# Performance work log

Hardware: AMD Instinct MI355X
Metric: run time of the kernel (lower is better)

The kernel has to match this reference:

```python
import jax, jax.numpy as jnp
import numpy as np

D = 1024      # d_model
E = 8         # num_experts
K = 2         # top_k
H = 4096      # expert_dim (bottleneck)
P = 256       # proj_dim
BATCH, SEQ = 2, 2048
CLAMP_MAX = float(np.log(1.0 / 0.01))
INIT_T = 0.5


def setup_inputs() -> dict:
    key = jax.random.key(0)
    ks = jax.random.split(key, 6)
    x = jax.random.normal(ks[0], (BATCH, SEQ, D), jnp.float32)
    # cosine projector (nn.Linear default init ~ U(-1/sqrt(D), 1/sqrt(D)))
    lim = 1.0 / np.sqrt(D)
    Wp = jax.random.uniform(ks[1], (P, D), jnp.float32, -lim, lim)
    bp = jnp.zeros((P,), jnp.float32)
    sim = 0.01 * jax.random.normal(ks[2], (P, E), jnp.float32)
    temp = jnp.full((1,), np.log(1.0 / INIT_T), jnp.float32)
    # RepAdapter 1x1 convs == linear layers; xavier_uniform, zero bias
    bA = float(np.sqrt(6.0 / (D + H)))
    A = jax.random.uniform(ks[3], (E, H, D), jnp.float32, -bA, bA)
    a_bias = jnp.zeros((E, H), jnp.float32)
    Bw = jax.random.uniform(ks[4], (E, D, H), jnp.float32, -bA, bA)
    b_bias = jnp.zeros((E, D), jnp.float32)
    return dict(x=x, Wp=Wp, bp=bp, sim=sim, temp=temp, A=A, a_bias=a_bias, Bw=Bw, b_bias=b_bias)


def reference(x, Wp, bp, sim, temp, A, a_bias, Bw, b_bias):
    B, S, d = x.shape
    e = sim.shape[1]
    xf = x.reshape(-1, d)                                  # [T, D]
    # cosine gate
    proj = xf @ Wp.T + bp                                  # [T, P]
    projn = proj / jnp.maximum(jnp.linalg.norm(proj, axis=1, keepdims=True), 1e-12)
    simn = sim / jnp.maximum(jnp.linalg.norm(sim, axis=0, keepdims=True), 1e-12)
    scale = jnp.exp(jnp.minimum(temp, CLAMP_MAX))          # [1]
    gate_probs = jax.nn.softmax((projn @ simn) * scale, axis=-1)   # [T, E]
    topv, topi = jax.lax.top_k(gate_probs, K)              # [T, K]
    topv = topv / (topv.sum(axis=-1, keepdims=True) + 1e-8)
    # per-token per-expert combine weight
    w = jnp.sum(topv[:, :, None] * jax.nn.one_hot(topi, e, dtype=x.dtype), axis=1)  # [T, E]

    # experts: y_e(x) = x + B_e(A_e x + a_e) + b_e (no nonlinearity); combine weighted
    def body(acc, params):
        Ae, ab, Be, bb, we = params
        h = xf @ Ae.T + ab                                 # [T, H]
        f = h @ Be.T + bb                                  # [T, D]
        return acc + we[:, None] * (xf + f), None

    out, _ = jax.lax.scan(body, jnp.zeros_like(xf), (A, a_bias, Bw, b_bias, w.T))
    out = out.reshape(B, S, d)

    frac = gate_probs.mean(axis=0)                         # expert_fractions
    aux_loss = jnp.sum((frac - 1.0 / e) ** 2)
    usage = jnp.bincount(topi.reshape(-1), length=e).astype(jnp.float32)
    return out, aux_loss, frac, usage
```

## Files before the change

kernel.cpp:

```cpp
#include <hip/hip_runtime.h>
#include <stdint.h>


typedef __attribute__((ext_vector_type(4))) float floatx4;
typedef __attribute__((ext_vector_type(8))) short shortx8;
typedef unsigned short ushort_t;

#define T_TOKENS 4096
#define D_DIM    1024
#define E_EXP    8
#define H_DIM    4096
#define P_DIM    256
#define ROWS_PAD 9344
#define MBLK     73

__device__ __forceinline__ ushort_t f2bf(float f) {
  union { float f; unsigned int u; } c; c.f = f;
  unsigned int u = c.u;
  unsigned int r = u + 0x7FFFu + ((u >> 16) & 1u);
  return (ushort_t)(r >> 16);
}

__device__ __forceinline__ void stage16(const ushort_t* g, ushort_t* l) {
  __builtin_amdgcn_global_load_lds(
      (__attribute__((address_space(1))) void*)(uintptr_t)g,
      (__attribute__((address_space(3))) void*)l, 16, 0, 0);
}

__global__ __launch_bounds__(256) void k_cvt(const float* __restrict__ src,
                                             ushort_t* __restrict__ dst, int n4) {
  int g = blockIdx.x * 256 + threadIdx.x;
  if (g >= n4) return;
  floatx4 v = ((const floatx4*)src)[g];
  ushort4 o; o.x = f2bf(v.x); o.y = f2bf(v.y); o.z = f2bf(v.z); o.w = f2bf(v.w);
  ((ushort4*)dst)[g] = o;
}

__global__ __launch_bounds__(256) void k_small_init(int* counts, int* cursor,
                                                    float* frac_sum, int* row2tok) {
  int g = blockIdx.x * 256 + threadIdx.x;
  if (g < 8) { counts[g] = 0; cursor[g] = 0; frac_sum[g] = 0.f; }
  if (g < ROWS_PAD) row2tok[g] = -1;
}

__global__ __launch_bounds__(256) void k_proj(const float* __restrict__ x,
                                              const float* __restrict__ Wp,
                                              const float* __restrict__ bp,
                                              float* __restrict__ proj) {
  __shared__ float Wc[256 * 36];
  __shared__ float Xc[16 * 36];
  int tid = threadIdx.x;
  int t0 = blockIdx.x * 16;
  int cg = tid & 31, tg = tid >> 5;
  floatx4 acc[2][8];
#pragma unroll
  for (int a = 0; a < 2; a++)
#pragma unroll
    for (int b = 0; b < 8; b++) acc[a][b] = (floatx4){0.f, 0.f, 0.f, 0.f};
  for (int kc = 0; kc < 32; ++kc) {
    int k0 = kc * 32;
    __syncthreads();
#pragma unroll
    for (int it = 0; it < 8; ++it) {
      int f = it * 256 + tid;
      int j = f >> 3, kk = (f & 7) << 2;
      floatx4 v = *(const floatx4*)(Wp + j * 1024 + k0 + kk);
      *(floatx4*)(Wc + j * 36 + kk) = v;
    }
    if (tid < 128) {
      int t = tid >> 3, kk = (tid & 7) << 2;
      floatx4 v = *(const floatx4*)(x + (size_t)(t0 + t) * 1024 + k0 + kk);
      *(floatx4*)(Xc + t * 36 + kk) = v;
    }
    __syncthreads();
#pragma unroll
    for (int k4 = 0; k4 < 8; ++k4) {
      floatx4 xv[2], wv[8];
#pragma unroll
      for (int tt = 0; tt < 2; tt++) xv[tt] = *(floatx4*)(Xc + (tg * 2 + tt) * 36 + k4 * 4);
#pragma unroll
      for (int jj = 0; jj < 8; jj++) wv[jj] = *(floatx4*)(Wc + (cg + jj * 32) * 36 + k4 * 4);
#pragma unroll
      for (int tt = 0; tt < 2; tt++)
#pragma unroll
        for (int jj = 0; jj < 8; jj++) acc[tt][jj] += xv[tt] * wv[jj];
    }
  }
#pragma unroll
  for (int tt = 0; tt < 2; tt++)
#pragma unroll
    for (int jj = 0; jj < 8; jj++) {
      floatx4 a = acc[tt][jj];
      float s = (a.x + a.y) + (a.z + a.w);
      int t = t0 + tg * 2 + tt, j = cg + jj * 32;
      proj[t * 256 + j] = s + bp[j];
    }
}

__global__ __launch_bounds__(128) void k_gate(const float* __restrict__ proj,
                                              const float* __restrict__ sim,
                                              const float* __restrict__ temp,
                                              int* __restrict__ topi, float* __restrict__ wslot,
                                              float* __restrict__ swsum,
                                              float* __restrict__ frac_sum, int* __restrict__ counts) {
  __shared__ float simT[8][256];
  __shared__ float snorm[8];
  __shared__ float fracs[8];
  __shared__ int cnts[8];
  int tid = threadIdx.x;
  for (int i = tid; i < 2048; i += 128) { int p = i >> 3, e = i & 7; simT[e][p] = sim[i]; }
  if (tid < 8) { fracs[tid] = 0.f; cnts[tid] = 0; }
  __syncthreads();
  if (tid < 8) {
    float s = 0.f;
    for (int p = 0; p < 256; p++) { float v = simT[tid][p]; s += v * v; }
    snorm[tid] = fmaxf(sqrtf(s), 1e-12f);
  }
  __syncthreads();
  int t = blockIdx.x * 128 + tid;
  floatx4 n4 = (floatx4){0.f, 0.f, 0.f, 0.f};
  floatx4 d4[8];
#pragma unroll
  for (int e = 0; e < 8; e++) d4[e] = (floatx4){0.f, 0.f, 0.f, 0.f};
  const floatx4* pr = (const floatx4*)(proj + t * 256);
  for (int k4 = 0; k4 < 64; ++k4) {
    floatx4 p = pr[k4];
    n4 += p * p;
#pragma unroll
    for (int e = 0; e < 8; e++) d4[e] += p * *(const floatx4*)(&simT[e][k4 * 4]);
  }
  float nrm = fmaxf(sqrtf((n4.x + n4.y) + (n4.z + n4.w)), 1e-12f);
  float scale = expf(fminf(temp[0], 4.6051701859880914f));
  float pe[8];
  float mx = -1e30f;
#pragma unroll
  for (int e = 0; e < 8; e++) {
    float d = (d4[e].x + d4[e].y) + (d4[e].z + d4[e].w);
    pe[e] = d / (nrm * snorm[e]) * scale;
    mx = fmaxf(mx, pe[e]);
  }
  float sum = 0.f;
#pragma unroll
  for (int e = 0; e < 8; e++) { pe[e] = expf(pe[e] - mx); sum += pe[e]; }
#pragma unroll
  for (int e = 0; e < 8; e++) pe[e] /= sum;
  int i0 = 0;
#pragma unroll
  for (int e = 1; e < 8; e++) if (pe[e] > pe[i0]) i0 = e;
  int i1 = (i0 == 0) ? 1 : 0;
#pragma unroll
  for (int e = 0; e < 8; e++) if (e != i1 && e != i0 && pe[e] > pe[i1]) i1 = e;
  float v0 = pe[i0], v1 = pe[i1];
  float s2 = v0 + v1 + 1e-8f;
  float w0 = v0 / s2, w1 = v1 / s2;
  topi[t * 2] = i0; topi[t * 2 + 1] = i1;
  wslot[t * 2] = w0; wslot[t * 2 + 1] = w1;
  swsum[t] = w0 + w1;
#pragma unroll
  for (int e = 0; e < 8; e++) atomicAdd(&fracs[e], pe[e]);
  atomicAdd(&cnts[i0], 1); atomicAdd(&cnts[i1], 1);
  __syncthreads();
  if (tid < 8) { atomicAdd(&frac_sum[tid], fracs[tid]); atomicAdd(&counts[tid], cnts[tid]); }
}

__global__ void k_scan(const int* __restrict__ counts, const float* __restrict__ frac_sum,
                       int* __restrict__ offsets, int* __restrict__ blk2e,
                       float* __restrict__ out_tail) {
  __shared__ int offs[9];
  if (threadIdx.x == 0) {
    int off = 0;
    for (int e = 0; e < 8; e++) { offs[e] = off; off += ((counts[e] + 127) >> 7) << 7; }
    offs[8] = off;
    for (int e = 0; e < 9; e++) offsets[e] = offs[e];
    float aux = 0.f;
    for (int e = 0; e < 8; e++) { float fr = frac_sum[e] / 4096.f; aux += (fr - 0.125f) * (fr - 0.125f); }
    out_tail[0] = aux;
  }
  __syncthreads();
  int tid = threadIdx.x;
  if (tid < MBLK) {
    int r = tid * 128, e = -1;
    for (int q = 0; q < 8; q++) if (r >= offs[q] && r < offs[q + 1]) e = q;
    blk2e[tid] = e;
  }
  if (tid < 8) {
    out_tail[1 + tid] = frac_sum[tid] / 4096.f;
    out_tail[9 + tid] = (float)counts[tid];
  }
}

__global__ __launch_bounds__(256) void k_assign(const int* __restrict__ topi,
                                                const float* __restrict__ wslot,
                                                const int* __restrict__ offsets,
                                                int* __restrict__ cursor,
                                                int* __restrict__ row2tok, float* __restrict__ roww) {
  int g = blockIdx.x * 256 + threadIdx.x;
  if (g >= 8192) return;
  int t = g >> 1;
  int e = topi[g];
  int pos = atomicAdd(&cursor[e], 1);
  int r = offsets[e] + pos;
  row2tok[r] = t;
  roww[r] = wslot[g];
}

__global__ __launch_bounds__(64) void k_gather(const float* __restrict__ x,
                                               const int* __restrict__ row2tok,
                                               ushort_t* __restrict__ xg) {
  int r = blockIdx.x;
  int t = row2tok[r];
  ushort4* dst = (ushort4*)(xg + (size_t)r * 1024);
  if (t < 0) {
    ushort4 z; z.x = z.y = z.z = z.w = 0;
    for (int i = threadIdx.x; i < 256; i += 64) dst[i] = z;
  } else {
    const floatx4* src = (const floatx4*)(x + (size_t)t * 1024);
    for (int i = threadIdx.x; i < 256; i += 64) {
      floatx4 v = src[i];
      ushort4 o; o.x = f2bf(v.x); o.y = f2bf(v.y); o.z = f2bf(v.z); o.w = f2bf(v.w);
      dst[i] = o;
    }
  }
}

__global__ __launch_bounds__(256) void k_init_out(const float* __restrict__ x,
                                                  const float* __restrict__ swsum,
                                                  float* __restrict__ out) {
  int g = blockIdx.x * 256 + threadIdx.x;
  float s = swsum[g >> 8];
  floatx4 v = ((const floatx4*)x)[g];
  ((floatx4*)out)[g] = v * s;
}

__global__ __launch_bounds__(256) void k_gemm(const ushort_t* __restrict__ Aop0,
                                              const ushort_t* __restrict__ Wall,
                                              const float* __restrict__ bias,
                                              const int* __restrict__ blk2e,
                                              int K, int N,
                                              ushort_t* __restrict__ hout,
                                              float* __restrict__ outp,
                                              const int* __restrict__ row2tok,
                                              const float* __restrict__ roww) {
  int e = blk2e[blockIdx.y];
  if (e < 0) return;
  int rb = blockIdx.y, nb = blockIdx.x;
  const ushort_t* Aop = Aop0 + (size_t)rb * 128 * K;
  const ushort_t* Bop = Wall + (size_t)e * N * K + (size_t)nb * 128 * K;
  __shared__ ushort_t As[4096], Bs[4096];
  int tid = threadIdx.x, lane = tid & 63, wv = tid >> 6;
  int l15 = lane & 15, q = lane >> 4;
  int wm = (wv & 1) << 6, wn = (wv >> 1) << 6;
  floatx4 acc[4][4];
#pragma unroll
  for (int i = 0; i < 4; i++)
#pragma unroll
    for (int j = 0; j < 4; j++) acc[i][j] = (floatx4){0.f, 0.f, 0.f, 0.f};
  int c0 = tid, c1 = 256 + tid;
  size_t sa0 = (size_t)(c0 >> 2) * K + ((c0 & 3) << 3);
  size_t sa1 = (size_t)(c1 >> 2) * K + ((c1 & 3) << 3);
  ushort_t* lA0 = As + wv * 512;
  ushort_t* lA1 = As + 2048 + wv * 512;
  ushort_t* lB0 = Bs + wv * 512;
  ushort_t* lB1 = Bs + 2048 + wv * 512;
  int ksteps = K >> 5;
  for (int ks = 0; ks < ksteps; ++ks) {
    const ushort_t* Ak = Aop + ks * 32;
    const ushort_t* Bk = Bop + ks * 32;
    stage16(Ak + sa0, lA0);
    stage16(Ak + sa1, lA1);
    stage16(Bk + sa0, lB0);
    stage16(Bk + sa1, lB1);
    __syncthreads();
    shortx8 af[4], bfv[4];
#pragma unroll
    for (int i = 0; i < 4; i++) af[i] = *(const shortx8*)(As + ((wm + i * 16 + l15) << 5) + (q << 3));
#pragma unroll
    for (int i = 0; i < 4; i++) bfv[i] = *(const shortx8*)(Bs + ((wn + i * 16 + l15) << 5) + (q << 3));
#pragma unroll
    for (int i = 0; i < 4; i++)
#pragma unroll
      for (int j = 0; j < 4; j++)
        acc[i][j] = __builtin_amdgcn_mfma_f32_16x16x32_bf16(af[i], bfv[j], acc[i][j], 0, 0, 0);
    __syncthreads();
  }
  const float* be = bias + (size_t)e * N + (size_t)nb * 128;
  if (hout) {
    ushort_t* hp = hout + (size_t)(rb * 128) * N + nb * 128;
#pragma unroll
    for (int j = 0; j < 4; j++) {
      int n = wn + j * 16 + l15;
      float bv = be[n];
#pragma unroll
      for (int i = 0; i < 4; i++)
#pragma unroll
        for (int r = 0; r < 4; r++) {
          int m = wm + i * 16 + (q << 2) + r;
          hp[(size_t)m * N + n] = f2bf(acc[i][j][r] + bv);
        }
    }
  } else {
#pragma unroll
    for (int j = 0; j < 4; j++) {
      int n = wn + j * 16 + l15;
      float bv = be[n];
#pragma unroll
      for (int i = 0; i < 4; i++)
#pragma unroll
        for (int r = 0; r < 4; r++) {
          int m = wm + i * 16 + (q << 2) + r;
          int grow = rb * 128 + m;
          int tok = row2tok[grow];
          if (tok >= 0) {
            float v = (acc[i][j][r] + bv) * roww[grow];
            atomicAdd(outp + (size_t)tok * 1024 + nb * 128 + n, v);
          }
        }
    }
  }
}

extern "C" void kernel_launch(void* const* d_in, const int* in_sizes, int n_in,
                              void* d_out, int out_size, void* d_ws, size_t ws_size,
                              hipStream_t stream) {
  (void)in_sizes; (void)n_in; (void)out_size; (void)ws_size;
  const float* x      = (const float*)d_in[0];
  const float* Wp     = (const float*)d_in[1];
  const float* bp     = (const float*)d_in[2];
  const float* sim    = (const float*)d_in[3];
  const float* temp   = (const float*)d_in[4];
  const float* A      = (const float*)d_in[5];
  const float* a_bias = (const float*)d_in[6];
  const float* Bw     = (const float*)d_in[7];
  const float* b_bias = (const float*)d_in[8];
  float* out = (float*)d_out;

  char* ws = (char*)d_ws;
  ushort_t* Abf    = (ushort_t*)(ws);
  ushort_t* Bbf    = (ushort_t*)(ws + 67108864);
  ushort_t* xg     = (ushort_t*)(ws + 134217728);
  ushort_t* h      = (ushort_t*)(ws + 153354240);
  float*    proj   = (float*)   (ws + 229900288);
  int*      topi   = (int*)     (ws + 234094592);
  float*    wslot  = (float*)   (ws + 234127360);
  float*    swsum  = (float*)   (ws + 234160128);
  int*      row2tok= (int*)     (ws + 234176512);
  float*    roww   = (float*)   (ws + 234213888);
  int*      counts = (int*)     (ws + 234251264);
  int*      cursor = (int*)     (ws + 234251296);
  int*      offsets= (int*)     (ws + 234251328);
  int*      blk2e  = (int*)     (ws + 234251392);
  float*    fracs  = (float*)   (ws + 234251712);

  k_cvt<<<32768, 256, 0, stream>>>(A,  Abf, 8388608);
  k_cvt<<<32768, 256, 0, stream>>>(Bw, Bbf, 8388608);
  k_small_init<<<37, 256, 0, stream>>>(counts, cursor, fracs, row2tok);
  k_proj<<<256, 256, 0, stream>>>(x, Wp, bp, proj);
  k_gate<<<32, 128, 0, stream>>>(proj, sim, temp, topi, wslot, swsum, fracs, counts);
  k_scan<<<1, 128, 0, stream>>>(counts, fracs, offsets, blk2e, out + 4194304);
  k_assign<<<32, 256, 0, stream>>>(topi, wslot, offsets, cursor, row2tok, roww);
  k_gather<<<ROWS_PAD, 64, 0, stream>>>(x, row2tok, xg);
  k_init_out<<<4096, 256, 0, stream>>>(x, swsum, out);
  k_gemm<<<dim3(32, MBLK), 256, 0, stream>>>(xg, Abf, a_bias, blk2e, 1024, 4096,
                                             h, nullptr, nullptr, nullptr);
  k_gemm<<<dim3(8, MBLK), 256, 0, stream>>>(h, Bbf, b_bias, blk2e, 4096, 1024,
                                            nullptr, out, row2tok, roww);
}
```

Before: 871.3 us.

## Deepen GEMM K-tile to 64 with XOR-swizzled LDS and split-K second GEMM

```diff
diff --git a/kernel.cpp b/kernel.cpp
--- a/kernel.cpp
+++ b/kernel.cpp
@@ -244,9 +244,11 @@
   int e = blk2e[blockIdx.y];
   if (e < 0) return;
   int rb = blockIdx.y, nb = blockIdx.x;
-  const ushort_t* Aop = Aop0 + (size_t)rb * 128 * K;
-  const ushort_t* Bop = Wall + (size_t)e * N * K + (size_t)nb * 128 * K;
-  __shared__ ushort_t As[4096], Bs[4096];
+  int Kslice = K / gridDim.z;
+  int kbase = blockIdx.z * Kslice;
+  const ushort_t* Aop = Aop0 + (size_t)rb * 128 * K + kbase;
+  const ushort_t* Bop = Wall + (size_t)e * N * K + (size_t)nb * 128 * K + kbase;
+  __shared__ ushort_t As[8192], Bs[8192];
   int tid = threadIdx.x, lane = tid & 63, wv = tid >> 6;
   int l15 = lane & 15, q = lane >> 4;
   int wm = (wv & 1) << 6, wn = (wv >> 1) << 6;
@@ -255,32 +257,40 @@
   for (int i = 0; i < 4; i++)
 #pragma unroll
     for (int j = 0; j < 4; j++) acc[i][j] = (floatx4){0.f, 0.f, 0.f, 0.f};
-  int c0 = tid, c1 = 256 + tid;
-  size_t sa0 = (size_t)(c0 >> 2) * K + ((c0 & 3) << 3);
-  size_t sa1 = (size_t)(c1 >> 2) * K + ((c1 & 3) << 3);
-  ushort_t* lA0 = As + wv * 512;
-  ushort_t* lA1 = As + 2048 + wv * 512;
-  ushort_t* lB0 = Bs + wv * 512;
-  ushort_t* lB1 = Bs + 2048 + wv * 512;
-  int ksteps = K >> 5;
+  int row0 = tid >> 3;
+  int swz  = (tid & 7) ^ (row0 & 7);
+  size_t sa = (size_t)row0 * K + (size_t)(swz << 3);
+  int ldsoff = wv * 512;
+  int ksteps = Kslice >> 6;
   for (int ks = 0; ks < ksteps; ++ks) {
-    const ushort_t* Ak = Aop + ks * 32;
-    const ushort_t* Bk = Bop + ks * 32;
-    stage16(Ak + sa0, lA0);
-    stage16(Ak + sa1, lA1);
-    stage16(Bk + sa0, lB0);
-    stage16(Bk + sa1, lB1);
+    const ushort_t* Ak = Aop + ks * 64;
+    const ushort_t* Bk = Bop + ks * 64;
+#pragma unroll
+    for (int r = 0; r < 4; ++r) {
+      stage16(Ak + sa + (size_t)(r * 32) * K, As + r * 2048 + ldsoff);
+      stage16(Bk + sa + (size_t)(r * 32) * K, Bs + r * 2048 + ldsoff);
+    }
     __syncthreads();
-    shortx8 af[4], bfv[4];
-#pragma unroll
-    for (int i = 0; i < 4; i++) af[i] = *(const shortx8*)(As + ((wm + i * 16 + l15) << 5) + (q << 3));
-#pragma unroll
-    for (int i = 0; i < 4; i++) bfv[i] = *(const shortx8*)(Bs + ((wn + i * 16 + l15) << 5) + (q << 3));
-#pragma unroll
-    for (int i = 0; i < 4; i++)
-#pragma unroll
-      for (int j = 0; j < 4; j++)
-        acc[i][j] = __builtin_amdgcn_mfma_f32_16x16x32_bf16(af[i], bfv[j], acc[i][j], 0, 0, 0);
+#pragma unroll
+    for (int s = 0; s < 2; ++s) {
+      int cw = (s << 2) + q;
+      shortx8 af[4], bfv[4];
+#pragma unroll
+      for (int i = 0; i < 4; i++) {
+        int row = wm + i * 16 + l15;
+        af[i] = *(const shortx8*)(As + (row << 6) + ((cw ^ (row & 7)) << 3));
+      }
+#pragma unroll
+      for (int j = 0; j < 4; j++) {
+        int row = wn + j * 16 + l15;
+        bfv[j] = *(const shortx8*)(Bs + (row << 6) + ((cw ^ (row & 7)) << 3));
+      }
+#pragma unroll
+      for (int i = 0; i < 4; i++)
+#pragma unroll
+        for (int j = 0; j < 4; j++)
+          acc[i][j] = __builtin_amdgcn_mfma_f32_16x16x32_bf16(af[i], bfv[j], acc[i][j], 0, 0, 0);
+    }
     __syncthreads();
   }
   const float* be = bias + (size_t)e * N + (size_t)nb * 128;
@@ -299,10 +309,11 @@
         }
     }
   } else {
+    bool addb = (blockIdx.z == 0);
 #pragma unroll
     for (int j = 0; j < 4; j++) {
       int n = wn + j * 16 + l15;
-      float bv = be[n];
+      float bv = addb ? be[n] : 0.f;
 #pragma unroll
       for (int i = 0; i < 4; i++)
 #pragma unroll
@@ -360,8 +371,8 @@
   k_assign<<<32, 256, 0, stream>>>(topi, wslot, offsets, cursor, row2tok, roww);
   k_gather<<<ROWS_PAD, 64, 0, stream>>>(x, row2tok, xg);
   k_init_out<<<4096, 256, 0, stream>>>(x, swsum, out);
-  k_gemm<<<dim3(32, MBLK), 256, 0, stream>>>(xg, Abf, a_bias, blk2e, 1024, 4096,
-                                             h, nullptr, nullptr, nullptr);
-  k_gemm<<<dim3(8, MBLK), 256, 0, stream>>>(h, Bbf, b_bias, blk2e, 4096, 1024,
-                                            nullptr, out, row2tok, roww);
-}
+  k_gemm<<<dim3(32, MBLK, 1), 256, 0, stream>>>(xg, Abf, a_bias, blk2e, 1024, 4096,
+                                                h, nullptr, nullptr, nullptr);
+  k_gemm<<<dim3(8, MBLK, 4), 256, 0, stream>>>(h, Bbf, b_bias, blk2e, 4096, 1024,
+                                               nullptr, out, row2tok, roww);
+}
```

Measured after the change: 857.4 us. About the same (-1.6%).
